# Optimization experiments

Hardware: AMD Instinct MI355X
Metric: run time of the kernel (lower is better)

Reference implementation:

```python
import jax, jax.numpy as jnp
import numpy as np

DIM = 128      # d_msa
HEADS = 8
DH = 64        # dim_head
INNER = HEADS * DH  # 512
R = 64         # tie_attn_dim (MSA rows)
N = 512        # residues
DPAIR = 128
LN_EPS = 1e-5


def _layernorm(x, g, b):
    mu = jnp.mean(x, axis=-1, keepdims=True)
    var = jnp.mean((x - mu) ** 2, axis=-1, keepdims=True)
    return (x - mu) * jax.lax.rsqrt(var + LN_EPS) * g + b


def setup_inputs() -> dict:
    key = jax.random.key(0)
    ks = jax.random.split(key, 12)
    s = 0.02
    return {
        "x": jax.random.normal(ks[0], (R, N, DIM), jnp.float32),
        "pair_bias": jax.random.normal(ks[1], (1, N, N, DPAIR), jnp.float32),
        "Wq": jax.random.normal(ks[2], (DIM, INNER), jnp.float32) * s,
        "Wkv": jax.random.normal(ks[3], (DIM, 2 * INNER), jnp.float32) * s,
        "Wo": jax.random.normal(ks[4], (INNER, DIM), jnp.float32) * s,
        "bo": jnp.zeros((DIM,), jnp.float32),
        "ln_g": jnp.ones((DPAIR,), jnp.float32),
        "ln_b": jnp.zeros((DPAIR,), jnp.float32),
        "Wpair": jax.random.normal(ks[5], (DPAIR, HEADS), jnp.float32) * s,
        "Wsq": jax.random.normal(ks[6], (DIM, DIM), jnp.float32) * s,
        "bsq": jnp.zeros((DIM,), jnp.float32),
        "Wsk": jax.random.normal(ks[7], (DIM, DIM), jnp.float32) * s,
        "bsk": jnp.zeros((DIM,), jnp.float32),
        "tie_attn_dim": R,
    }


def reference(x, pair_bias, Wq, Wkv, Wo, bo, ln_g, ln_b, Wpair, Wsq, bsq, Wsk, bsk, tie_attn_dim):
    r = tie_attn_dim
    br, n, dim = x.shape
    b = br // r
    h, dh = HEADS, DH
    dsw = dim // h  # per-head dim inside PositionalWiseWeight

    # projections: (b*r, n, inner) -> (b, r, h, n, dh)
    q = (x @ Wq).reshape(b, r, n, h, dh).transpose(0, 1, 3, 2, 4)
    kv = x @ Wkv
    k, v = jnp.split(kv, 2, axis=-1)
    k = k.reshape(b, r, n, h, dh).transpose(0, 1, 3, 2, 4)
    v = v.reshape(b, r, n, h, dh).transpose(0, 1, 3, 2, 4)

    # soft tied row weights (PositionalWiseWeight): w[b, i(pos), h, r]
    m = x.reshape(b, r, n, dim)
    sq = (m[:, :1] @ Wsq + bsq).reshape(b, 1, n, h, dsw).transpose(0, 2, 3, 1, 4)  # b n h 1 d
    sk = (m @ Wsk + bsk).reshape(b, r, n, h, dsw).transpose(0, 2, 3, 1, 4)          # b n h r d
    wlog = jnp.einsum('bnhud,bnhrd->bnhr', sq, sk) / np.float32(np.sqrt(dsw))
    w = jax.nn.softmax(wlog, axis=-1)  # softmax over rows r

    # tied-row attention logits with soft weights
    scale = np.float32(dh) ** -0.5
    dots = jnp.einsum('bihr,brhid,brhjd->bhij', w, q, k) * scale

    # pair bias: LayerNorm + Linear(dim_pair -> heads), broadcast into logits
    pb = _layernorm(pair_bias, ln_g, ln_b) @ Wpair  # (b, i, j, h)
    dots = dots + pb.transpose(0, 3, 1, 2)

    attn = jax.nn.softmax(dots, axis=-1)  # (b, h, i, j)

    out = jnp.einsum('bhij,brhjd->brhid', attn, v)           # (b, r, h, n, dh)
    out = out.transpose(0, 1, 3, 2, 4).reshape(br, n, h * dh)
    out = out @ Wo + bo                                       # (b*r, n, dim)
    return out.reshape(1, br, n, dim)
```

## Files before the change

kernel.cpp:

```cpp
#include <hip/hip_runtime.h>
#include <hip/hip_bf16.h>

typedef unsigned short u16;
typedef unsigned int u32;
typedef __attribute__((ext_vector_type(8))) short short8;
typedef __attribute__((ext_vector_type(4))) float floatx4;

__device__ inline float bf2f(u16 u) { union { u32 i; float f; } v; v.i = ((u32)u) << 16; return v.f; }
__device__ inline u16 f2bf(float f) {
    union { float f; u32 i; } v; v.f = f;
    u32 lsb = (v.i >> 16) & 1u;
    v.i += 0x7fffu + lsb;
    return (u16)(v.i >> 16);
}

__device__ inline uint4 pack8(float4 a, float4 b) {
    uint4 q;
    q.x = (u32)f2bf(a.x) | ((u32)f2bf(a.y) << 16);
    q.y = (u32)f2bf(a.z) | ((u32)f2bf(a.w) << 16);
    q.z = (u32)f2bf(b.x) | ((u32)f2bf(b.y) << 16);
    q.w = (u32)f2bf(b.z) | ((u32)f2bf(b.w) << 16);
    return q;
}

__device__ inline void ld8(u16* dst, const float* src) {
    const float4 a = *(const float4*)src;
    const float4 b = *(const float4*)(src + 4);
    *(uint4*)dst = pack8(a, b);
}

__device__ inline void async16(u16* ldst, const u16* gsrc) {
    __builtin_amdgcn_global_load_lds((const __attribute__((address_space(1))) u32*)gsrc,
                                     (__attribute__((address_space(3))) u32*)ldst, 16, 0, 0);
}

template <int N> __device__ inline void waitvm() {
    static_assert(N == 0 || N == 2 || N == 3 || N == 4 || N == 6 || N == 8, "unsupported vmcnt");
    if constexpr (N == 0) asm volatile("s_waitcnt vmcnt(0)" ::: "memory");
    if constexpr (N == 2) asm volatile("s_waitcnt vmcnt(2)" ::: "memory");
    if constexpr (N == 3) asm volatile("s_waitcnt vmcnt(3)" ::: "memory");
    if constexpr (N == 4) asm volatile("s_waitcnt vmcnt(4)" ::: "memory");
    if constexpr (N == 6) asm volatile("s_waitcnt vmcnt(6)" ::: "memory");
    if constexpr (N == 8) asm volatile("s_waitcnt vmcnt(8)" ::: "memory");
}
__device__ inline void barrier_raw() {
    asm volatile("s_barrier" ::: "memory");
    __builtin_amdgcn_sched_barrier(0);
}
__device__ inline void waitlgkm0() {
    asm volatile("s_waitcnt lgkmcnt(0)" ::: "memory");
    __builtin_amdgcn_sched_barrier(0);
}

template <int BM, int BN, class Epi>
__global__ __launch_bounds__(256) void gemm_nt(const u16* __restrict__ A, const u16* __restrict__ B,
                                               long sAz, long sBz, int lda, int ldb, int K, int zlog, Epi epi)
{
    constexpr int AELE = BM * 32, BELE = BN * 32;
    constexpr int SLOT = AELE + BELE;
    constexpr int IA = BM / 64, IB = BN / 64;
    constexpr int PW = IA + IB;
    constexpr bool STAGE = Epi::chunked;
    static_assert(!STAGE || BN == 128, "chunked epilogue assumes BN=128");
    constexpr int LDC = BN + 4;
    constexpr size_t RB = sizeof(u16) * 3 * (size_t)SLOT;
    constexpr size_t EBR = STAGE ? sizeof(float) * 64 * (size_t)LDC : 0;
    constexpr size_t EBV = (STAGE && Epi::kv) ? sizeof(float) * 128 * 68 : 0;
    constexpr size_t EB = EBR > EBV ? EBR : EBV;
    constexpr size_t LB = RB > EB ? RB : EB;
    __shared__ __align__(16) char smem[LB];
    u16* lds = (u16*)smem;
    const int tid  = threadIdx.x;
    const int lane = tid & 63;
    const int wave = tid >> 6;

    int bx = blockIdx.x, by = blockIdx.y, bz = blockIdx.z;
    if constexpr (Epi::xswz) {
        int gx = gridDim.x, gy = gridDim.y;
        int n = gx * gy * (int)gridDim.z;
        int o = (bz * gy + by) * gx + bx;
        int wg = (o & 7) * (n >> 3) + (o >> 3);
        bx = wg % gx; int t = wg / gx; by = t % gy; bz = t / gy;
    }
    const int zh = bz >> zlog;
    const int zk = bz & ((1 << zlog) - 1);
    if constexpr (Epi::ylim >= 0) {
        if (zh != 0 && by >= Epi::ylim) return;
    }
    const long row0 = (long)by * BM;
    const long col0 = (long)bx * BN;
    const u16* Ab = A + (long)zh * sAz + row0 * lda + (long)zk * K;
    const u16* Bb = B + (long)zh * sBz + col0 * ldb + (long)zk * K;
    constexpr int WM = BM / 2, WN = BN / 2, TM = WM / 16, TN = WN / 16;
    const int wm = (wave >> 1) * WM;
    const int wn = (wave & 1) * WN;
    const int l15 = lane & 15;
    const int quad = lane >> 4;
    const int swz = (l15 >> 1) & 3;

    floatx4 acc[TM][TN];
#pragma unroll
    for (int i = 0; i < TM; i++)
#pragma unroll
        for (int j = 0; j < TN; j++) acc[i][j] = (floatx4){0.f, 0.f, 0.f, 0.f};

    auto stage = [&](int slot, int ki) {
        const int k0 = ki << 5;
        u16* base = lds + slot * SLOT;
#pragma unroll
        for (int i2 = 0; i2 < IA; i2++) {
            int s = wave * (IA * 64) + i2 * 64 + lane;
            int r = s >> 2, c = (s & 3) ^ ((r >> 1) & 3);
            async16(base + (wave * (IA * 64) + i2 * 64) * 8, Ab + (long)r * lda + k0 + c * 8);
        }
        u16* bbase = base + AELE;
#pragma unroll
        for (int i2 = 0; i2 < IB; i2++) {
            int s = wave * (IB * 64) + i2 * 64 + lane;
            int r = s >> 2, c = (s & 3) ^ ((r >> 1) & 3);
            async16(bbase + (wave * (IB * 64) + i2 * 64) * 8, Bb + (long)r * ldb + k0 + c * 8);
        }
    };

    auto compute = [&](int slot) {
        const u16* As = lds + slot * SLOT;
        const u16* Bs = As + AELE;
        short8 af[TM], bfr[TN];
#pragma unroll
        for (int t = 0; t < TM; t++)
            af[t] = *(const short8*)(As + (wm + t * 16 + l15) * 32 + (quad ^ swz) * 8);
#pragma unroll
        for (int t = 0; t < TN; t++)
            bfr[t] = *(const short8*)(Bs + (wn + t * 16 + l15) * 32 + (quad ^ swz) * 8);
        waitlgkm0();
#pragma unroll
        for (int i = 0; i < TM; i++)
#pragma unroll
            for (int j = 0; j < TN; j++)
                acc[i][j] = __builtin_amdgcn_mfma_f32_16x16x32_bf16(af[i], bfr[j], acc[i][j], 0, 0, 0);
    };

    const int nIter = K >> 5;
    stage(0, 0);
    stage(1, 1);
    int s0 = 0, s1 = 1, s2 = 2;
    for (int i = 0; i + 2 < nIter; i++) {
        waitvm<PW>();
        barrier_raw();
        stage(s2, i + 2);
        compute(s0);
        int t = s0; s0 = s1; s1 = s2; s2 = t;
    }
    waitvm<PW>(); barrier_raw(); compute(s0);
    waitvm<0>();  barrier_raw(); compute(s1);

    if constexpr (STAGE) {
        float* cs = (float*)smem;
        constexpr int NP = BM / 64;
        bool vtile = false;
        if constexpr (Epi::kv) vtile = (col0 >= Epi::vbase);
#pragma unroll
        for (int p = 0; p < NP; p++) {
            __syncthreads();
            if (!vtile) {
                if ((wm >> 6) == p) {
                    const int lr0 = wm & 63;
#pragma unroll
                    for (int i = 0; i < TM; i++)
#pragma unroll
                        for (int j = 0; j < TN; j++)
#pragma unroll
                            for (int r = 0; r < 4; r++)
                                cs[(lr0 + i * 16 + quad * 4 + r) * LDC + wn + j * 16 + l15] = acc[i][j][r];
                }
                __syncthreads();
                constexpr int CPT = (64 * BN) / (256 * 8);
#pragma unroll
                for (int k = 0; k < CPT; k++) {
                    int g = k * 256 + tid;
                    int row = g >> 4, c8 = (g & 15) * 8;
                    const float* pp = cs + row * LDC + c8;
                    float4 a = *(const float4*)pp;
                    float4 b = *(const float4*)(pp + 4);
                    epi.chunk(zh, zk, (int)row0 + p * 64 + row, (int)col0 + c8, a, b);
                }
            }
            if constexpr (Epi::kv) {
                if (vtile) {
                    if ((wm >> 6) == p) {
                        const int lr0 = wm & 63;
#pragma unroll
                        for (int i = 0; i < TM; i++)
#pragma unroll
                            for (int j = 0; j < TN; j++)
                                *(float4*)&cs[(wn + j * 16 + l15) * 68 + lr0 + i * 16 + quad * 4] =
                                    (float4){acc[i][j][0], acc[i][j][1], acc[i][j][2], acc[i][j][3]};
                    }
                    __syncthreads();
#pragma unroll
                    for (int k = 0; k < 4; k++) {
                        int q = k * 256 + tid;
                        int colL = q >> 3, rg = q & 7;
                        const float* pp = cs + colL * 68 + rg * 8;
                        float4 a = *(const float4*)pp;
                        float4 b = *(const float4*)(pp + 4);
                        epi.vchunk(zh, (int)row0 + p * 64 + rg * 8, (int)col0 + colL, a, b);
                    }
                }
            }
        }
    } else {
#pragma unroll
        for (int i = 0; i < TM; i++)
#pragma unroll
            for (int j = 0; j < TN; j++)
#pragma unroll
                for (int r = 0; r < 4; r++) {
                    int row = (int)row0 + wm + i * 16 + quad * 4 + r;
                    int col = (int)col0 + wn + j * 16 + l15;
                    epi(zh, zk, row, col, acc[i][j][r]);
                }
    }
}

struct EpiSkSq {
    static constexpr bool chunked = true;
    static constexpr bool kv = false;
    static constexpr bool xswz = false;
    static constexpr int vbase = 0;
    static constexpr int ylim = 8;
    u16* sk; u16* sq; const float* bsk; const float* bsq;
    __device__ void chunk(int zh, int, int row, int col, float4 a, float4 b) const {
        const float* bias = zh ? bsq : bsk;
        u16* C = zh ? sq : sk;
        const float4* bp = (const float4*)(bias + col);
        float4 b0 = bp[0], b1 = bp[1];
        a.x += b0.x; a.y += b0.y; a.z += b0.z; a.w += b0.w;
        b.x += b1.x; b.y += b1.y; b.z += b1.z; b.w += b1.w;
        *(uint4*)(C + (long)row * 128 + col) = pack8(a, b);
    }
};
struct EpiQKV {
    static constexpr bool chunked = true;
    static constexpr bool kv = true;
    static constexpr bool xswz = true;
    static constexpr int vbase = 1024;
    static constexpr int ylim = -1;
    u16* Qw; u16* Kp; u16* Vt; const float* w;
    __device__ void chunk(int, int, int row, int col, float4 a, float4 b) const {
        int r = row >> 9, i = row & 511;
        if (col < 512) {
            int h = col >> 6, d = col & 63;
            float s = w[((long)(i * 8 + h)) * 64 + r] * 0.125f;
            a.x *= s; a.y *= s; a.z *= s; a.w *= s;
            b.x *= s; b.y *= s; b.z *= s; b.w *= s;
            *(uint4*)(Qw + (long)h * 2097152 + (long)i * 4096 + r * 64 + d) = pack8(a, b);
        } else {
            int c = col - 512, h = c >> 6, d = c & 63;
            *(uint4*)(Kp + (long)h * 2097152 + (long)i * 4096 + r * 64 + d) = pack8(a, b);
        }
    }
    __device__ void vchunk(int, int row8, int col, float4 a, float4 b) const {
        int r = row8 >> 9, j0 = row8 & 511;
        int c = col - vbase, h = c >> 6, d = c & 63;
        *(uint4*)(Vt + (long)h * 2097152 + ((long)r * 64 + d) * 512 + j0) = pack8(a, b);
    }
};
struct EpiDotsAtomic {
    static constexpr bool chunked = false;
    static constexpr bool kv = false;
    static constexpr bool xswz = false;
    static constexpr int vbase = 0;
    static constexpr int ylim = -1;
    float* pbdots;
    __device__ void operator()(int zh, int, int row, int col, float v) const {
        atomicAdd(pbdots + (long)zh * 262144 + (long)row * 512 + col, v);
    }
};
struct EpiDotsPart {
    static constexpr bool chunked = true;
    static constexpr bool kv = false;
    static constexpr bool xswz = true;
    static constexpr int vbase = 0;
    static constexpr int ylim = -1;
    float* pbd; float* parts;
    __device__ void chunk(int zh, int zk, int row, int col, float4 a, float4 b) const {
        long idx = (long)zh * 262144 + (long)row * 512 + col;
        if (zk == 0) {
            float4* p = (float4*)(pbd + idx);
            float4 p0 = p[0], p1 = p[1];
            p0.x += a.x; p0.y += a.y; p0.z += a.z; p0.w += a.w;
            p1.x += b.x; p1.y += b.y; p1.z += b.z; p1.w += b.w;
            p[0] = p0; p[1] = p1;
        } else {
            float4* p = (float4*)(parts + (long)(zk - 1) * 2097152 + idx);
            p[0] = a; p[1] = b;
        }
    }
};
struct EpiPV {
    static constexpr bool chunked = true;
    static constexpr bool kv = false;
    static constexpr bool xswz = true;
    static constexpr int vbase = 0;
    static constexpr int ylim = -1;
    u16* O2;
    __device__ void chunk(int zh, int, int row, int col, float4 a, float4 b) const {
        int r = col >> 6, d = col & 63;
        *(uint4*)(O2 + ((long)r * 512 + row) * 512 + zh * 64 + d) = pack8(a, b);
    }
};
struct EpiOut {
    static constexpr bool chunked = true;
    static constexpr bool kv = false;
    static constexpr bool xswz = false;
    static constexpr int vbase = 0;
    static constexpr int ylim = -1;
    float* out; const float* bo;
    __device__ void chunk(int, int, int row, int col, float4 a, float4 b) const {
        const float4* bp = (const float4*)(bo + col);
        float4 b0 = bp[0], b1 = bp[1];
        a.x += b0.x; a.y += b0.y; a.z += b0.z; a.w += b0.w;
        b.x += b1.x; b.y += b1.y; b.z += b1.z; b.w += b1.w;
        float4* o = (float4*)(out + (long)row * 128 + col);
        o[0] = a; o[1] = b;
    }
};

__device__ inline void trans_dev(const float* __restrict__ src, u16* __restrict__ dst,
                                 int R, int C, int bx, int by, int tid)
{
    __shared__ u16 t[32][33];
    int c0 = bx * 32, r0 = by * 32;
    int tx = tid & 31, ty = tid >> 5;
#pragma unroll
    for (int i = 0; i < 32; i += 8) t[ty + i][tx] = f2bf(src[(long)(r0 + ty + i) * C + c0 + tx]);
    __syncthreads();
#pragma unroll
    for (int i = 0; i < 32; i += 8) dst[(long)(c0 + ty + i) * R + r0 + tx] = t[tx][ty + i];
}

__global__ __launch_bounds__(256) void prep_kernel(
    const float* __restrict__ x, u16* __restrict__ xbf,
    const float* __restrict__ Wq, u16* __restrict__ WqT,
    const float* __restrict__ Wkv, u16* __restrict__ WkvT,
    const float* __restrict__ Wsk, u16* __restrict__ WskT,
    const float* __restrict__ Wsq, u16* __restrict__ WsqT,
    const float* __restrict__ Wo, u16* __restrict__ WoT,
    const float* __restrict__ g, const float* __restrict__ b,
    const float* __restrict__ Wp, float* __restrict__ Wg, float* __restrict__ SB)
{
    int gb = blockIdx.x, tid = threadIdx.x;
    if (gb < 2048) { long i = ((long)gb * 256 + tid) * 8; ld8(xbf + i, x + i); return; }
    gb -= 2048;
    if (gb < 64)  { trans_dev(Wq,  WqT,  128, 512,  gb & 15, gb >> 4, tid); return; }
    gb -= 64;
    if (gb < 128) { trans_dev(Wkv, WkvT, 128, 1024, gb & 31, gb >> 5, tid); return; }
    gb -= 128;
    if (gb < 16)  { trans_dev(Wsk, WskT, 128, 128,  gb & 3,  gb >> 2, tid); return; }
    gb -= 16;
    if (gb < 16)  { trans_dev(Wsq, WsqT, 128, 128,  gb & 3,  gb >> 2, tid); return; }
    gb -= 16;
    if (gb < 64)  { trans_dev(Wo,  WoT,  512, 128,  gb & 3,  gb >> 2, tid); return; }
    for (int t = tid; t < 1024; t += 256) Wg[t] = g[t >> 3] * Wp[t];
    if (tid < 16) {
        int h = tid & 7;
        const float* src = (tid < 8) ? g : b;
        float s = 0.f;
        for (int c = 0; c < 128; c++) s += src[c] * Wp[c * 8 + h];
        SB[tid] = s;
    }
}

__global__ __launch_bounds__(256) void rowweight_kernel(const u16* __restrict__ sk, const u16* __restrict__ sq,
                                                        float* __restrict__ w)
{
    int wid = blockIdx.x * 4 + (threadIdx.x >> 6);
    int lane = threadIdx.x & 63;
    int i = wid >> 3, h = wid & 7;
    const u16* sqp = sq + i * 128 + h * 16;
    const u16* skp = sk + ((long)lane * 512 + i) * 128 + h * 16;
    float dot = 0.f;
#pragma unroll
    for (int c = 0; c < 16; c++) dot += bf2f(sqp[c]) * bf2f(skp[c]);
    float logit = dot * 0.25f;
    float m = logit;
#pragma unroll
    for (int o = 32; o > 0; o >>= 1) m = fmaxf(m, __shfl_xor(m, o));
    float e = __expf(logit - m);
    float ssum = e;
#pragma unroll
    for (int o = 32; o > 0; o >>= 1) ssum += __shfl_xor(ssum, o);
    w[(long)wid * 64 + lane] = e / ssum;
}

__global__ __launch_bounds__(256) void pb_kernel(const float* __restrict__ pair, const float* __restrict__ Wg,
                                                 const float* __restrict__ SB, float* __restrict__ pb)
{
    __shared__ __align__(16) float Ls[64 * 132];
    __shared__ float sWg[1024];
    __shared__ float sSB[16];
    int tid = threadIdx.x;
    for (int t = tid; t < 1024; t += 256) sWg[t] = Wg[t];
    if (tid < 16) sSB[tid] = SB[tid];
    long base = (long)blockIdx.x * 8192;
    const float4* src = (const float4*)(pair + base);
#pragma unroll
    for (int k = 0; k < 8; k++) {
        int e = tid + k * 256;
        float4 v = src[e];
        int r = e >> 5, c = (e & 31) << 2;
        *(float4*)(&Ls[r * 132 + c]) = v;
    }
    __syncthreads();
    int r = tid >> 2, sub = tid & 3;
    const float* row = &Ls[r * 132];
    float sum = 0.f, sqs = 0.f;
#pragma unroll
    for (int k = 0; k < 8; k++) {
        float4 v = *(const float4*)(&row[sub * 32 + k * 4]);
        sum += v.x + v.y + v.z + v.w;
        sqs += v.x * v.x + v.y * v.y + v.z * v.z + v.w * v.w;
    }
    sum += __shfl_xor(sum, 1); sqs += __shfl_xor(sqs, 1);
    sum += __shfl_xor(sum, 2); sqs += __shfl_xor(sqs, 2);
    float mu = sum * (1.f / 128.f);
    float var = sqs * (1.f / 128.f) - mu * mu;
    float rstd = rsqrtf(var + 1e-5f);
    int h0 = sub * 2;
    float a0 = 0.f, a1 = 0.f;
#pragma unroll
    for (int k = 0; k < 32; k++) {
        float4 v = *(const float4*)(&row[k * 4]);
        int c = k * 4;
        a0 += v.x * sWg[c * 8 + h0]     + v.y * sWg[(c + 1) * 8 + h0]
            + v.z * sWg[(c + 2) * 8 + h0] + v.w * sWg[(c + 3) * 8 + h0];
        a1 += v.x * sWg[c * 8 + h0 + 1]     + v.y * sWg[(c + 1) * 8 + h0 + 1]
            + v.z * sWg[(c + 2) * 8 + h0 + 1] + v.w * sWg[(c + 3) * 8 + h0 + 1];
    }
    long idx = (long)blockIdx.x * 64 + r;
    pb[(long)h0 * 262144 + idx]       = rstd * (a0 - mu * sSB[h0])     + sSB[8 + h0];
    pb[(long)(h0 + 1) * 262144 + idx] = rstd * (a1 - mu * sSB[h0 + 1]) + sSB[8 + h0 + 1];
}

__global__ __launch_bounds__(256) void softmax_kernel(const float* __restrict__ dots,
                                                      const float* __restrict__ parts, int np,
                                                      u16* __restrict__ attn)
{
    int row = blockIdx.x * 4 + (threadIdx.x >> 6);
    int lane = threadIdx.x & 63;
    long base = (long)row * 512;
    const float* dp = dots + base;
    float v[8];
#pragma unroll
    for (int k = 0; k < 8; k++) v[k] = dp[k * 64 + lane];
    for (int t = 0; t < np; t++) {
        const float* pp = parts + (long)t * 2097152 + base;
#pragma unroll
        for (int k = 0; k < 8; k++) v[k] += pp[k * 64 + lane];
    }
    float m = v[0];
#pragma unroll
    for (int k = 1; k < 8; k++) m = fmaxf(m, v[k]);
#pragma unroll
    for (int o = 32; o > 0; o >>= 1) m = fmaxf(m, __shfl_xor(m, o));
    float s = 0.f;
#pragma unroll
    for (int k = 0; k < 8; k++) { v[k] = __expf(v[k] - m); s += v[k]; }
#pragma unroll
    for (int o = 32; o > 0; o >>= 1) s += __shfl_xor(s, o);
    float inv = 1.f / s;
    u16* ap = attn + (long)row * 512;
#pragma unroll
    for (int k = 0; k < 8; k++) ap[k * 64 + lane] = f2bf(v[k] * inv);
}

extern "C" void kernel_launch(void* const* d_in, const int* in_sizes, int n_in,
                              void* d_out, int out_size, void* d_ws, size_t ws_size,
                              hipStream_t stream)
{
    const float* x    = (const float*)d_in[0];
    const float* pair = (const float*)d_in[1];
    const float* Wq   = (const float*)d_in[2];
    const float* Wkv  = (const float*)d_in[3];
    const float* Wo   = (const float*)d_in[4];
    const float* bo   = (const float*)d_in[5];
    const float* lng  = (const float*)d_in[6];
    const float* lnb  = (const float*)d_in[7];
    const float* Wp   = (const float*)d_in[8];
    const float* Wsq  = (const float*)d_in[9];
    const float* bsq  = (const float*)d_in[10];
    const float* Wsk  = (const float*)d_in[11];
    const float* bsk  = (const float*)d_in[12];
    float* out = (float*)d_out;

    char* ws = (char*)d_ws;
    size_t off = 0;
    auto alloc = [&](size_t bytes) -> char* {
        char* p = ws + off; off += (bytes + 255) & ~(size_t)255; return p;
    };
    u16* WqT  = (u16*)alloc(512 * 128 * 2);
    u16* WkvT = (u16*)alloc(1024 * 128 * 2);
    u16* WskT = (u16*)alloc(128 * 128 * 2);
    u16* WsqT = (u16*)alloc(128 * 128 * 2);
    u16* WoT  = (u16*)alloc(128 * 512 * 2);
    u16* xbf  = (u16*)alloc((size_t)32768 * 128 * 2);
    u16* sk   = (u16*)alloc((size_t)32768 * 128 * 2);
    u16* sq   = (u16*)alloc(512 * 128 * 2);
    float* w  = (float*)alloc((size_t)4096 * 64 * 4);
    float* Wg = (float*)alloc(1024 * 4);
    float* SB = (float*)alloc(16 * 4);
    u16* bufA = (u16*)alloc((size_t)8 * 512 * 4096 * 2);
    u16* bufB = (u16*)alloc((size_t)8 * 512 * 4096 * 2);
    u16* Vt   = (u16*)alloc((size_t)8 * 4096 * 512 * 2);
    float* pbd = (float*)alloc((size_t)8 * 512 * 512 * 4);
    float* parts = (float*)alloc((size_t)3 * 2097152 * 4);
    const bool useParts = (off <= ws_size);
    u16* attn = sk;

    dim3 blk(256);

    prep_kernel<<<dim3(2337), blk, 0, stream>>>(x, xbf, Wq, WqT, Wkv, WkvT,
                                                Wsk, WskT, Wsq, WsqT, Wo, WoT,
                                                lng, lnb, Wp, Wg, SB);

    gemm_nt<64, 128, EpiSkSq><<<dim3(1, 512, 2), blk, 0, stream>>>(
        xbf, WskT, 0, 16384, 128, 128, 128, 0, EpiSkSq{sk, sq, bsk, bsq});
    rowweight_kernel<<<dim3(1024), blk, 0, stream>>>(sk, sq, w);

    pb_kernel<<<dim3(4096), blk, 0, stream>>>(pair, Wg, SB, pbd);

    gemm_nt<128, 128, EpiQKV><<<dim3(12, 256, 1), blk, 0, stream>>>(
        xbf, WqT, 0, 0, 128, 128, 128, 0, EpiQKV{bufA, bufB, Vt, w});

    if (useParts) {
        gemm_nt<128, 128, EpiDotsPart><<<dim3(4, 4, 32), blk, 0, stream>>>(
            bufA, bufB, 2097152, 2097152, 4096, 4096, 1024, 2, EpiDotsPart{pbd, parts});
        softmax_kernel<<<dim3(1024), blk, 0, stream>>>(pbd, parts, 3, attn);
    } else {
        gemm_nt<128, 128, EpiDotsAtomic><<<dim3(4, 4, 64), blk, 0, stream>>>(
            bufA, bufB, 2097152, 2097152, 4096, 4096, 512, 3, EpiDotsAtomic{pbd});
        softmax_kernel<<<dim3(1024), blk, 0, stream>>>(pbd, pbd, 0, attn);
    }

    gemm_nt<128, 128, EpiPV><<<dim3(32, 4, 8), blk, 0, stream>>>(
        attn, Vt, 262144, 2097152, 512, 512, 512, 0, EpiPV{bufB});

    gemm_nt<64, 128, EpiOut><<<dim3(1, 512, 1), blk, 0, stream>>>(
        bufB, WoT, 0, 0, 512, 512, 512, 0, EpiOut{out, bo});
}
```

Before: 365.9 us.

## Merge pair-bias LayerNorm kernel into QKV GEMM launch as extra blocks

```diff
diff --git a/kernel.cpp b/kernel.cpp
--- a/kernel.cpp
+++ b/kernel.cpp
@@ -53,8 +53,19 @@
 }
 
 template <int BM, int BN, class Epi>
-__global__ __launch_bounds__(256) void gemm_nt(const u16* __restrict__ A, const u16* __restrict__ B,
-                                               long sAz, long sBz, int lda, int ldb, int K, int zlog, Epi epi)
+constexpr size_t gemm_lds_bytes() {
+    size_t SLOT = (size_t)(BM * 32 + BN * 32);
+    size_t RB = 2 * 3 * SLOT;
+    size_t EBR = Epi::chunked ? 4 * 64 * (size_t)(BN + 4) : 0;
+    size_t EBV = (Epi::chunked && Epi::kv) ? 4 * 128 * 68 : 0;
+    size_t EB = EBR > EBV ? EBR : EBV;
+    return RB > EB ? RB : EB;
+}
+
+template <int BM, int BN, class Epi>
+__device__ __forceinline__ void gemm_body(char* smem, const u16* __restrict__ A, const u16* __restrict__ B,
+                                          long sAz, long sBz, int lda, int ldb, int K, int zlog, Epi epi,
+                                          int o, int gx, int gy, int gz)
 {
     constexpr int AELE = BM * 32, BELE = BN * 32;
     constexpr int SLOT = AELE + BELE;
@@ -63,24 +74,18 @@
     constexpr bool STAGE = Epi::chunked;
     static_assert(!STAGE || BN == 128, "chunked epilogue assumes BN=128");
     constexpr int LDC = BN + 4;
-    constexpr size_t RB = sizeof(u16) * 3 * (size_t)SLOT;
-    constexpr size_t EBR = STAGE ? sizeof(float) * 64 * (size_t)LDC : 0;
-    constexpr size_t EBV = (STAGE && Epi::kv) ? sizeof(float) * 128 * 68 : 0;
-    constexpr size_t EB = EBR > EBV ? EBR : EBV;
-    constexpr size_t LB = RB > EB ? RB : EB;
-    __shared__ __align__(16) char smem[LB];
     u16* lds = (u16*)smem;
     const int tid  = threadIdx.x;
     const int lane = tid & 63;
     const int wave = tid >> 6;
 
-    int bx = blockIdx.x, by = blockIdx.y, bz = blockIdx.z;
+    int bx, by, bz;
     if constexpr (Epi::xswz) {
-        int gx = gridDim.x, gy = gridDim.y;
-        int n = gx * gy * (int)gridDim.z;
-        int o = (bz * gy + by) * gx + bx;
+        int n = gx * gy * gz;
         int wg = (o & 7) * (n >> 3) + (o >> 3);
         bx = wg % gx; int t = wg / gx; by = t % gy; bz = t / gy;
+    } else {
+        bx = o % gx; int t = o / gx; by = t % gy; bz = t / gy;
     }
     const int zh = bz >> zlog;
     const int zk = bz & ((1 << zlog) - 1);
@@ -221,6 +226,16 @@
                     epi(zh, zk, row, col, acc[i][j][r]);
                 }
     }
+}
+
+template <int BM, int BN, class Epi>
+__global__ __launch_bounds__(256) void gemm_nt(const u16* __restrict__ A, const u16* __restrict__ B,
+                                               long sAz, long sBz, int lda, int ldb, int K, int zlog, Epi epi)
+{
+    __shared__ __align__(16) char smem[gemm_lds_bytes<BM, BN, Epi>()];
+    int o = ((int)blockIdx.z * gridDim.y + blockIdx.y) * gridDim.x + blockIdx.x;
+    gemm_body<BM, BN, Epi>(smem, A, B, sAz, sBz, lda, ldb, K, zlog, epi,
+                           o, gridDim.x, gridDim.y, gridDim.z);
 }
 
 struct EpiSkSq {
@@ -327,6 +342,73 @@
     }
 };
 
+__device__ __forceinline__ void pb_body(char* smem, const float* __restrict__ pair,
+                                        const float* __restrict__ Wg, const float* __restrict__ SB,
+                                        float* __restrict__ pb, int bid)
+{
+    float* Ls  = (float*)smem;
+    float* sWg = Ls + 64 * 132;
+    float* sSB = sWg + 1024;
+    int tid = threadIdx.x;
+    for (int t = tid; t < 1024; t += 256) sWg[t] = Wg[t];
+    if (tid < 16) sSB[tid] = SB[tid];
+    long base = (long)bid * 8192;
+    const float4* src = (const float4*)(pair + base);
+#pragma unroll
+    for (int k = 0; k < 8; k++) {
+        int e = tid + k * 256;
+        float4 v = src[e];
+        int r = e >> 5, c = (e & 31) << 2;
+        *(float4*)(&Ls[r * 132 + c]) = v;
+    }
+    __syncthreads();
+    int r = tid >> 2, sub = tid & 3;
+    const float* row = &Ls[r * 132];
+    float sum = 0.f, sqs = 0.f;
+#pragma unroll
+    for (int k = 0; k < 8; k++) {
+        float4 v = *(const float4*)(&row[sub * 32 + k * 4]);
+        sum += v.x + v.y + v.z + v.w;
+        sqs += v.x * v.x + v.y * v.y + v.z * v.z + v.w * v.w;
+    }
+    sum += __shfl_xor(sum, 1); sqs += __shfl_xor(sqs, 1);
+    sum += __shfl_xor(sum, 2); sqs += __shfl_xor(sqs, 2);
+    float mu = sum * (1.f / 128.f);
+    float var = sqs * (1.f / 128.f) - mu * mu;
+    float rstd = rsqrtf(var + 1e-5f);
+    int h0 = sub * 2;
+    float a0 = 0.f, a1 = 0.f;
+#pragma unroll
+    for (int k = 0; k < 32; k++) {
+        float4 v = *(const float4*)(&row[k * 4]);
+        int c = k * 4;
+        a0 += v.x * sWg[c * 8 + h0]     + v.y * sWg[(c + 1) * 8 + h0]
+            + v.z * sWg[(c + 2) * 8 + h0] + v.w * sWg[(c + 3) * 8 + h0];
+        a1 += v.x * sWg[c * 8 + h0 + 1]     + v.y * sWg[(c + 1) * 8 + h0 + 1]
+            + v.z * sWg[(c + 2) * 8 + h0 + 1] + v.w * sWg[(c + 3) * 8 + h0 + 1];
+    }
+    long idx = (long)bid * 64 + r;
+    pb[(long)h0 * 262144 + idx]       = rstd * (a0 - mu * sSB[h0])     + sSB[8 + h0];
+    pb[(long)(h0 + 1) * 262144 + idx] = rstd * (a1 - mu * sSB[h0 + 1]) + sSB[8 + h0 + 1];
+}
+
+__global__ __launch_bounds__(256) void qkvpb_kernel(
+    const u16* __restrict__ xbf, const u16* __restrict__ WqT,
+    u16* Qw, u16* Kp, u16* Vt, const float* __restrict__ w,
+    const float* __restrict__ pair, const float* __restrict__ Wg,
+    const float* __restrict__ SB, float* __restrict__ pbd)
+{
+    constexpr size_t LB = gemm_lds_bytes<128, 128, EpiQKV>();
+    __shared__ __align__(16) char smem[LB];
+    int gb = blockIdx.x;
+    if (gb < 3072) {
+        gemm_body<128, 128, EpiQKV>(smem, xbf, WqT, 0, 0, 128, 128, 128, 0,
+                                    EpiQKV{Qw, Kp, Vt, w}, gb, 12, 256, 1);
+    } else {
+        pb_body(smem, pair, Wg, SB, pbd, gb - 3072);
+    }
+}
+
 __device__ inline void trans_dev(const float* __restrict__ src, u16* __restrict__ dst,
                                  int R, int C, int bx, int by, int tid)
 {
@@ -392,55 +474,6 @@
 #pragma unroll
     for (int o = 32; o > 0; o >>= 1) ssum += __shfl_xor(ssum, o);
     w[(long)wid * 64 + lane] = e / ssum;
-}
-
-__global__ __launch_bounds__(256) void pb_kernel(const float* __restrict__ pair, const float* __restrict__ Wg,
-                                                 const float* __restrict__ SB, float* __restrict__ pb)
-{
-    __shared__ __align__(16) float Ls[64 * 132];
-    __shared__ float sWg[1024];
-    __shared__ float sSB[16];
-    int tid = threadIdx.x;
-    for (int t = tid; t < 1024; t += 256) sWg[t] = Wg[t];
-    if (tid < 16) sSB[tid] = SB[tid];
-    long base = (long)blockIdx.x * 8192;
-    const float4* src = (const float4*)(pair + base);
-#pragma unroll
-    for (int k = 0; k < 8; k++) {
-        int e = tid + k * 256;
-        float4 v = src[e];
-        int r = e >> 5, c = (e & 31) << 2;
-        *(float4*)(&Ls[r * 132 + c]) = v;
-    }
-    __syncthreads();
-    int r = tid >> 2, sub = tid & 3;
-    const float* row = &Ls[r * 132];
-    float sum = 0.f, sqs = 0.f;
-#pragma unroll
-    for (int k = 0; k < 8; k++) {
-        float4 v = *(const float4*)(&row[sub * 32 + k * 4]);
-        sum += v.x + v.y + v.z + v.w;
-        sqs += v.x * v.x + v.y * v.y + v.z * v.z + v.w * v.w;
-    }
-    sum += __shfl_xor(sum, 1); sqs += __shfl_xor(sqs, 1);
-    sum += __shfl_xor(sum, 2); sqs += __shfl_xor(sqs, 2);
-    float mu = sum * (1.f / 128.f);
-    float var = sqs * (1.f / 128.f) - mu * mu;
-    float rstd = rsqrtf(var + 1e-5f);
-    int h0 = sub * 2;
-    float a0 = 0.f, a1 = 0.f;
-#pragma unroll
-    for (int k = 0; k < 32; k++) {
-        float4 v = *(const float4*)(&row[k * 4]);
-        int c = k * 4;
-        a0 += v.x * sWg[c * 8 + h0]     + v.y * sWg[(c + 1) * 8 + h0]
-            + v.z * sWg[(c + 2) * 8 + h0] + v.w * sWg[(c + 3) * 8 + h0];
-        a1 += v.x * sWg[c * 8 + h0 + 1]     + v.y * sWg[(c + 1) * 8 + h0 + 1]
-            + v.z * sWg[(c + 2) * 8 + h0 + 1] + v.w * sWg[(c + 3) * 8 + h0 + 1];
-    }
-    long idx = (long)blockIdx.x * 64 + r;
-    pb[(long)h0 * 262144 + idx]       = rstd * (a0 - mu * sSB[h0])     + sSB[8 + h0];
-    pb[(long)(h0 + 1) * 262144 + idx] = rstd * (a1 - mu * sSB[h0 + 1]) + sSB[8 + h0 + 1];
 }
 
 __global__ __launch_bounds__(256) void softmax_kernel(const float* __restrict__ dots,
@@ -528,10 +561,8 @@
         xbf, WskT, 0, 16384, 128, 128, 128, 0, EpiSkSq{sk, sq, bsk, bsq});
     rowweight_kernel<<<dim3(1024), blk, 0, stream>>>(sk, sq, w);
 
-    pb_kernel<<<dim3(4096), blk, 0, stream>>>(pair, Wg, SB, pbd);
-
-    gemm_nt<128, 128, EpiQKV><<<dim3(12, 256, 1), blk, 0, stream>>>(
-        xbf, WqT, 0, 0, 128, 128, 128, 0, EpiQKV{bufA, bufB, Vt, w});
+    qkvpb_kernel<<<dim3(7168), blk, 0, stream>>>(xbf, WqT, bufA, bufB, Vt, w,
+                                                 pair, Wg, SB, pbd);
 
     if (useParts) {
         gemm_nt<128, 128, EpiDotsPart><<<dim3(4, 4, 32), blk, 0, stream>>>(
```

Result: faster. 353.4 us (-3.4%).
